# Optimization experiments

Hardware: AMD Instinct MI355X
Metric: run time of the kernel (lower is better)

## Reference

```python
import jax, jax.numpy as jnp
from jax import lax
import numpy as np

WINDOW_SIZES = (1, 2, 3)


def _proj(x, w1, b1, w2, b2):
    # gated projection: sigmoid(Linear1) * tanh(Linear2)
    return jax.nn.sigmoid(x @ w1.T + b1) * jnp.tanh(x @ w2.T + b2)


def setup_inputs() -> dict:
    key = jax.random.key(0)
    ks = jax.random.split(key, 16)
    V, E, D = 50000, 1024, 1024
    N, La, Lq = 64, 512, 64
    s = 0.02  # weight scale to keep sigmoid/tanh unsaturated
    return {
        "data_q": jax.random.randint(ks[0], (Lq,), 0, V),
        "data_as": jax.random.randint(ks[1], (N, La), 0, V),
        "emb": jax.random.normal(ks[2], (V, E), jnp.float32),
        "w1": jax.random.normal(ks[3], (D, E), jnp.float32) * s,
        "b1": jnp.zeros((D,), jnp.float32),
        "w2": jax.random.normal(ks[4], (D, E), jnp.float32) * s,
        "b2": jnp.zeros((D,), jnp.float32),
        "cw1": jax.random.normal(ks[5], (D, D, 1), jnp.float32) * s,
        "cb1": jnp.zeros((D,), jnp.float32),
        "cw2": jax.random.normal(ks[6], (D, D, 2), jnp.float32) * s,
        "cb2": jnp.zeros((D,), jnp.float32),
        "cw3": jax.random.normal(ks[7], (D, D, 3), jnp.float32) * s,
        "cb3": jnp.zeros((D,), jnp.float32),
        "lin_w": jax.random.normal(ks[8], (D, 3 * D), jnp.float32) * s,
        "lin_b": jnp.zeros((D,), jnp.float32),
        "soft_w": jax.random.normal(ks[9], (1, D), jnp.float32) * s,
        "soft_b": jnp.zeros((1,), jnp.float32),
    }


def reference(data_q, data_as, emb, w1, b1, w2, b2,
              cw1, cb1, cw2, cb2, cw3, cb3, lin_w, lin_b, soft_w, soft_b):
    N, La = data_as.shape
    a_tok = data_as.reshape(-1)                     # [T] concatenated answers
    emb_a = emb[a_tok]                              # [T, E]
    emb_q = emb[data_q]                             # [Lq, E]
    pa = _proj(emb_a, w1, b1, w2, b2)               # [T, D]
    pq = _proj(emb_q, w1, b1, w2, b2)               # [Lq, D]

    # attention: M_r = q @ a^T ; alpha = softmax over question positions
    M = pq @ pa.T                                   # [Lq, T]
    alpha = jax.nn.softmax(M.T, axis=1)             # [T, Lq]
    Y = alpha @ pq                                  # [T, D]
    sim = pa * Y                                    # elementwise compare (mul)

    starts = jnp.arange(N) * La
    x = sim.T[None]                                 # [1, D, T]
    pools = []
    for w, cw, cb in zip(WINDOW_SIZES, (cw1, cw2, cw3), (cb1, cb2, cb3)):
        conv = lax.conv_general_dilated(
            x, cw, (1,), 'VALID',
            dimension_numbers=('NCW', 'OIW', 'NCW'))[0].T + cb  # [T-w+1, D]
        conv = jax.nn.relu(conv)
        # DMax: per-answer max over rows [start_k, start_k + La - w + 1)
        idx = starts[:, None] + jnp.arange(La - w + 1)[None, :]  # [N, La-w+1]
        pools.append(conv[idx].max(axis=1))          # [N, D]

    cat = jnp.concatenate(pools, axis=1)            # [N, 3D]
    h = jnp.tanh(cat @ lin_w.T + lin_b)             # [N, D]
    logits = (h @ soft_w.T + soft_b).reshape(-1)    # [N]
    return jax.nn.log_softmax(logits)
```

## Files before the change

### kernel.cpp

```cpp
#include <hip/hip_runtime.h>

#define DEV __device__ __forceinline__

typedef __bf16 bf16x8 __attribute__((ext_vector_type(8)));
typedef float f32x4 __attribute__((ext_vector_type(4)));
typedef unsigned short u16;
typedef u16 u16x4 __attribute__((ext_vector_type(4)));

constexpr int T_ANS = 32768;
constexpr int LQ    = 64;
constexpr int M_ALL = T_ANS + LQ;
constexpr int M_PAD = 33024;
constexpr int DIM   = 1024;

DEV u16 f2bf(float x) {
  unsigned u = __float_as_uint(x);
  return (u16)((u + 0x7FFFu + ((u >> 16) & 1u)) >> 16);
}
DEV float bf2f(u16 s) { return __uint_as_float(((unsigned)s) << 16); }

DEV void gl2lds16(const void* g, void* l) {
  __builtin_amdgcn_global_load_lds(
      (const __attribute__((address_space(1))) unsigned int*)g,
      (__attribute__((address_space(3))) unsigned int*)l, 16, 0, 0);
}

#define MF(A, B, C) __builtin_amdgcn_mfma_f32_16x16x32_bf16(A, B, C, 0, 0, 0)


#define LFC(BASE, OFF) (*(const bf16x8*)((BASE) + (OFF)))

#define STG(G, LT, R0) gl2lds16((G) + (R0) * 2048 + gOff, (LT) + (R0) * 128 + tidOff)

#define MQUAD(Q, a00, a01, a10, a11)                                                  \
    acc[2*(Q)][0]   = MF(a00, bb00, acc[2*(Q)][0]);                                   \
    acc[2*(Q)][1]   = MF(a00, bb10, acc[2*(Q)][1]);                                   \
    acc[2*(Q)][2]   = MF(a00, bb20, acc[2*(Q)][2]);                                   \
    acc[2*(Q)][3]   = MF(a00, bb30, acc[2*(Q)][3]);                                   \
    acc[2*(Q)+1][0] = MF(a10, bb00, acc[2*(Q)+1][0]);                                 \
    acc[2*(Q)+1][1] = MF(a10, bb10, acc[2*(Q)+1][1]);                                 \
    acc[2*(Q)+1][2] = MF(a10, bb20, acc[2*(Q)+1][2]);                                 \
    acc[2*(Q)+1][3] = MF(a10, bb30, acc[2*(Q)+1][3]);                                 \
    acc[2*(Q)][0]   = MF(a01, bb01, acc[2*(Q)][0]);                                   \
    acc[2*(Q)][1]   = MF(a01, bb11, acc[2*(Q)][1]);                                   \
    acc[2*(Q)][2]   = MF(a01, bb21, acc[2*(Q)][2]);                                   \
    acc[2*(Q)][3]   = MF(a01, bb31, acc[2*(Q)][3]);                                   \
    acc[2*(Q)+1][0] = MF(a11, bb01, acc[2*(Q)+1][0]);                                 \
    acc[2*(Q)+1][1] = MF(a11, bb11, acc[2*(Q)+1][1]);                                 \
    acc[2*(Q)+1][2] = MF(a11, bb21, acc[2*(Q)+1][2]);                                 \
    acc[2*(Q)+1][3] = MF(a11, bb31, acc[2*(Q)+1][3]);

#define BARW                                                                          \
    __builtin_amdgcn_s_barrier();                                                     \
    asm volatile("s_waitcnt lgkmcnt(0)" ::: "memory");                                \
    __builtin_amdgcn_sched_barrier(0);

#define VM0 asm volatile("s_waitcnt vmcnt(0)" ::: "memory"); __builtin_amdgcn_sched_barrier(0);

#define TILE(Ac0, Ac1, Bc0, Bc1, S0, S1, VMWv)                                        \
  {                                                    \
    bb00 = LFC(Bc0, 0);    bb01 = LFC(Bc1, 0);                                        \
    bb10 = LFC(Bc0, 2048); bb11 = LFC(Bc1, 2048);                                     \
    bb20 = LFC(Bc0, 4096); bb21 = LFC(Bc1, 4096);                                     \
    bb30 = LFC(Bc0, 6144); bb31 = LFC(Bc1, 6144);                                     \
    bf16x8 a00 = LFC(Ac0, 0),    a01 = LFC(Ac1, 0);                                   \
    bf16x8 a10 = LFC(Ac0, 2048), a11 = LFC(Ac1, 2048);                                \
    S0                                                                                \
    asm volatile("s_waitcnt lgkmcnt(8)" ::: "memory");                                \
    BARW                                                                              \
    __builtin_amdgcn_s_setprio(1); MQUAD(0, a00, a01, a10, a11)                       \
    __builtin_amdgcn_s_setprio(0);                                                    \
    __builtin_amdgcn_s_barrier();                                                     \
  }                                                                                   \
  {                                                                          \
    bf16x8 a00 = LFC(Ac0, 4096), a01 = LFC(Ac1, 4096);                                \
    bf16x8 a10 = LFC(Ac0, 6144), a11 = LFC(Ac1, 6144);                                \
    S1                                                                                \
    BARW                                                                              \
    __builtin_amdgcn_s_setprio(1); MQUAD(1, a00, a01, a10, a11)                       \
    __builtin_amdgcn_s_setprio(0);                                                    \
    __builtin_amdgcn_s_barrier();                                                     \
  }                                                                                   \
  {                                                                          \
    bf16x8 a00 = LFC(Ac0, 8192),  a01 = LFC(Ac1, 8192);                               \
    bf16x8 a10 = LFC(Ac0, 10240), a11 = LFC(Ac1, 10240);                              \
    BARW                                                                              \
    __builtin_amdgcn_s_setprio(1); MQUAD(2, a00, a01, a10, a11)                       \
    __builtin_amdgcn_s_setprio(0);                                                    \
    __builtin_amdgcn_s_barrier();                                                     \
  }                                                                                   \
  {                                                                          \
    bf16x8 a00 = LFC(Ac0, 12288), a01 = LFC(Ac1, 12288);                              \
    bf16x8 a10 = LFC(Ac0, 14336), a11 = LFC(Ac1, 14336);                              \
    BARW                                                                              \
    __builtin_amdgcn_s_setprio(1); MQUAD(3, a00, a01, a10, a11)                       \
    __builtin_amdgcn_s_setprio(0);                                                    \
    VMWv                                                                              \
    __builtin_amdgcn_s_barrier();                                                     \
  }

#define S_A(G, LT) { const char* g_ = (G); STG(g_, LT, 0); STG(g_, LT, 64); STG(g_, LT, 128); STG(g_, LT, 192); }

#define GEMM_PIPE(KT)                                                                 \
  f32x4 acc[8][4] = {};                                                               \
  bf16x8 bb00, bb01, bb10, bb11, bb20, bb21, bb30, bb31;                              \
  const int e_ = lane & 7, h_ = lane >> 4, blk0 = (h_ ^ e_) << 4, blk1 = ((h_ ^ e_) ^ 4) << 4; \
  const int rA0 = (wm + lr) * 128, rB0 = (wn + lr) * 128;                             \
  const char* A0c0 = lds + rA0 + blk0;          const char* A0c1 = lds + rA0 + blk1;  \
  const char* B0c0 = lds + 32768 + rB0 + blk0;  const char* B0c1 = lds + 32768 + rB0 + blk1; \
  const char* A1c0 = lds + 65536 + rA0 + blk0;  const char* A1c1 = lds + 65536 + rA0 + blk1; \
  const char* B1c0 = lds + 98304 + rB0 + blk0;  const char* B1c1 = lds + 98304 + rB0 + blk1; \
  char* ldsA0 = lds;          char* ldsB0 = lds + 32768;                              \
  char* ldsA1 = lds + 65536;  char* ldsB1 = lds + 98304;                              \
  const int tidOff = tid * 16;                                                        \
  const int gOff = (tid >> 3) * 2048 + (((tid & 7) ^ ((tid >> 3) & 7)) << 4);         \
  S_A(Ab(0), ldsA0) S_A(Bb(0), ldsB0)                                                 \
  VM0                                                                                 \
  __builtin_amdgcn_s_barrier();                                                       \
  for (int kp = 0; kp < (KT) / 2 - 1; ++kp) {                                         \
    const int k1 = 2 * kp + 1;                                                        \
    TILE(A0c0, A0c1, B0c0, B0c1, S_A(Ab(k1), ldsA1), S_A(Bb(k1), ldsB1), VM0)         \
    TILE(A1c0, A1c1, B1c0, B1c1, S_A(Ab(k1 + 1), ldsA0), S_A(Bb(k1 + 1), ldsB0), VM0) \
  }                                                                                   \
  TILE(A0c0, A0c1, B0c0, B0c1, S_A(Ab((KT) - 1), ldsA1), S_A(Bb((KT) - 1), ldsB1), VM0) \
  TILE(A1c0, A1c1, B1c0, B1c1, , , )


__global__ void cast4(const float* __restrict__ src, u16* __restrict__ dst, int n4) {
  int i = blockIdx.x * 256 + threadIdx.x;
  if (i < n4) {
    float4 v = ((const float4*)src)[i];
    u16x4 o = { f2bf(v.x), f2bf(v.y), f2bf(v.z), f2bf(v.w) };
    ((u16x4*)dst)[i] = o;
  }
}

template<int W>
__global__ void cast_conv_w(const float* __restrict__ src, u16* __restrict__ dst) {
  int i = blockIdx.x * 256 + threadIdx.x;
  if (i < 1024 * 1024) {
#pragma unroll
    for (int k = 0; k < W; ++k)
      dst[(size_t)k * (1024 * 1024) + i] = f2bf(src[(size_t)i * W + k]);
  }
}

__global__ void pack_w12(const float* __restrict__ w1, const float* __restrict__ w2,
                         u16* __restrict__ W12) {
  int i = blockIdx.x * 256 + threadIdx.x;
  if (i < 2048 * 1024) {
    int n2 = i >> 10, k = i & 1023;
    int j = n2 >> 4, m = n2 & 15;
    const float* src = (j & 1) ? w2 : w1;
    W12[i] = f2bf(src[(size_t)((j >> 1) * 16 + m) * 1024 + k]);
  }
}

__global__ void gather_cast(const int* __restrict__ dq, const int* __restrict__ das,
                            const float* __restrict__ emb, u16* __restrict__ X) {
  const int row = blockIdx.x;
  const int c   = threadIdx.x;
  size_t dsto = (size_t)row * DIM + c * 4;
  if (row >= M_ALL) {
    u16x4 z = {0, 0, 0, 0};
    *(u16x4*)(X + dsto) = z;
    return;
  }
  const int tok = (row < T_ANS) ? das[row] : dq[row - T_ANS];
  float4 v = ((const float4*)(emb + (size_t)tok * DIM))[c];
  u16x4 o = { f2bf(v.x), f2bf(v.y), f2bf(v.z), f2bf(v.w) };
  *(u16x4*)(X + dsto) = o;
}

__global__ void transpose_pq(const u16* __restrict__ pa, u16* __restrict__ pqT) {
  int i = blockIdx.x * 256 + threadIdx.x;
  int e = i >> 6, q = i & 63;
  pqT[i] = pa[(size_t)(T_ANS + q) * DIM + e];
}

__global__ void zero_pad_sim(u16* __restrict__ sim) {
  int i = blockIdx.x * 256 + threadIdx.x;
  if (i < 2 * DIM) sim[(size_t)T_ANS * DIM + i] = 0;
}

__global__ void cast_cat(const float* __restrict__ cat, u16* __restrict__ catb) {
  int i = blockIdx.x * 256 + threadIdx.x;
  if (i < 128 * 3072) {
    int row = i / 3072;
    catb[i] = (row < 64) ? f2bf(cat[i]) : (u16)0;
  }
}


__global__ __launch_bounds__(512, 1)
void proj_g(const u16* __restrict__ X, const u16* __restrict__ W12,
            const float* __restrict__ b1, const float* __restrict__ b2,
            u16* __restrict__ pa) {
  extern __shared__ char lds[];
  const int tid = threadIdx.x, lane = tid & 63;
  const int wid = tid >> 6;
  const int wm = (wid >> 2) * 128, wn = (wid & 3) * 64;
  const int lr = lane & 15;
  const int wg = ((int)blockIdx.x % 8) * 129 + (int)blockIdx.x / 8;
  const int tm = (wg >> 3) * 256, tn = (wg & 7) * 256;
  const char* Ag = (const char*)X + (size_t)tm * 2048;
  const char* Bg = (const char*)W12 + (size_t)tn * 2048;
  auto Ab = [&](int kt) { return Ag + ((kt & 15) << 7); };
  auto Bb = [&](int kt) { return Bg + ((kt & 15) << 7); };

  GEMM_PIPE(16)

  u16* cw = (u16*)lds;
  const int lg = (lane >> 4) * 4;
#pragma unroll
  for (int pp = 0; pp < 2; ++pp) {
    const int clocal = ((wn >> 5) + pp) * 16 + lr;
    const int col = (tn >> 1) + clocal;
    const float b1v = b1[col], b2v = b2[col];
#pragma unroll
    for (int mi = 0; mi < 8; ++mi)
#pragma unroll
      for (int r = 0; r < 4; ++r) {
        const int rowL = wm + mi * 16 + lg + r;
        const float x1 = acc[mi][2 * pp][r] + b1v;
        const float x2 = acc[mi][2 * pp + 1][r] + b2v;
        const float sg = 1.f / (1.f + __expf(-x1));
        const float th = 2.f / (1.f + __expf(-2.f * x2)) - 1.f;
        cw[rowL * 132 + clocal] = f2bf(sg * th);
      }
  }
  __syncthreads();
#pragma unroll
  for (int it = 0; it < 16; ++it) {
    const int cid = it * 512 + tid;
    const int rowL = cid >> 5, c4 = (cid & 31) * 4;
    u16x4 v = *(const u16x4*)(cw + rowL * 132 + c4);
    *(u16x4*)(pa + (size_t)(tm + rowL) * DIM + (tn >> 1) + c4) = v;
  }
}


template<int W>
__global__ __launch_bounds__(512, 1)
void conv_g(const u16* __restrict__ sim, const u16* __restrict__ Bw,
            const float* __restrict__ cb, float* __restrict__ cat) {
  extern __shared__ char lds[];
  const int tid = threadIdx.x, lane = tid & 63;
  const int wid = tid >> 6;
  const int wm = (wid >> 2) * 128, wn = (wid & 3) * 64;
  const int lr = lane & 15;
  const int wg = ((int)blockIdx.x % 8) * 64 + (int)blockIdx.x / 8;
  const int tm = (wg >> 2) * 256, tn = (wg & 3) * 256;
  const char* Ag = (const char*)sim + (size_t)tm * 2048;
  const char* Bg = (const char*)Bw + (size_t)tn * 2048;
  auto Ab = [&](int kt) { return Ag + (kt >> 4) * 2048 + ((kt & 15) << 7); };
  auto Bb = [&](int kt) { return Bg + (size_t)(kt >> 4) * 2097152 + ((kt & 15) << 7); };

  GEMM_PIPE(16 * W)

  const int lg = (lane >> 4) * 4;
  const int n = tm >> 9;
#pragma unroll
  for (int ni = 0; ni < 4; ++ni) {
    const int col = tn + wn + ni * 16 + lr;
    const float cbv = cb[col];
    float vmax = 0.f;
#pragma unroll
    for (int mi = 0; mi < 8; ++mi)
#pragma unroll
      for (int r = 0; r < 4; ++r) {
        const int t = tm + wm + mi * 16 + lg + r;
        float v = fmaxf(acc[mi][ni][r] + cbv, 0.f);
        if ((t & 511) > 512 - W) v = 0.f;
        vmax = fmaxf(vmax, v);
      }
    vmax = fmaxf(vmax, __shfl_xor(vmax, 16));
    vmax = fmaxf(vmax, __shfl_xor(vmax, 32));
    if (lane < 16)
      atomicMax((int*)&cat[(size_t)n * 3072 + (W - 1) * 1024 + col], __float_as_int(vmax));
  }
}


__global__ __launch_bounds__(256, 2)
void attn_s(const u16* __restrict__ pa, float* __restrict__ Spart) {
  __shared__ alignas(16) u16 sA[128 * 32];
  __shared__ alignas(16) u16 sB[64 * 32];
  const int tid = threadIdx.x, lane = tid & 63;
  const int tm = blockIdx.x * 128;
  const int kbase = blockIdx.y * 256;
  const int wid = tid >> 6;
  const int wm = (wid >> 1) * 64, wn = (wid & 1) * 32;
  const u16* pq = pa + (size_t)T_ANS * DIM;
  f32x4 acc[4][2] = {};
  for (int k0 = kbase; k0 < kbase + 256; k0 += 32) {
#pragma unroll
    for (int j = 0; j < 2; ++j) {
      const int f = tid * 16 + j * 4096;
      const int r = f >> 6, cb = f & 63;
      gl2lds16((const char*)pa + (size_t)(tm + r) * 2048 + k0 * 2 + cb, (char*)sA + f);
    }
    {
      const int f = tid * 16;
      const int r = f >> 6, cb = f & 63;
      gl2lds16((const char*)pq + (size_t)r * 2048 + k0 * 2 + cb, (char*)sB + f);
    }
    __syncthreads();
    const int lr = lane & 15, lk = (lane >> 4) * 8;
    bf16x8 af[4], bfr[2];
#pragma unroll
    for (int i = 0; i < 4; ++i)
      af[i] = *(const bf16x8*)(sA + (wm + i * 16 + lr) * 32 + lk);
#pragma unroll
    for (int i = 0; i < 2; ++i)
      bfr[i] = *(const bf16x8*)(sB + (wn + i * 16 + lr) * 32 + lk);
#pragma unroll
    for (int mi = 0; mi < 4; ++mi)
#pragma unroll
      for (int ni = 0; ni < 2; ++ni)
        acc[mi][ni] = MF(af[mi], bfr[ni], acc[mi][ni]);
    __syncthreads();
  }
  const int lr = lane & 15, lg = (lane >> 4) * 4;
  float* Sp = Spart + (size_t)blockIdx.y * (T_ANS * 64);
#pragma unroll
  for (int mi = 0; mi < 4; ++mi)
#pragma unroll
    for (int ni = 0; ni < 2; ++ni)
#pragma unroll
      for (int r = 0; r < 4; ++r) {
        const int row = tm + wm + mi * 16 + lg + r;
        const int col = wn + ni * 16 + lr;
        Sp[(size_t)row * 64 + col] = acc[mi][ni][r];
      }
}

__global__ void softmax64(const float* __restrict__ Spart, u16* __restrict__ alpha) {
  const int row = blockIdx.x * 4 + (threadIdx.x >> 6);
  const int lane = threadIdx.x & 63;
  const size_t o = (size_t)row * 64 + lane;
  float v = Spart[o] + Spart[(size_t)1 * T_ANS * 64 + o]
          + Spart[(size_t)2 * T_ANS * 64 + o] + Spart[(size_t)3 * T_ANS * 64 + o];
  float m = v;
#pragma unroll
  for (int o2 = 32; o2 > 0; o2 >>= 1) m = fmaxf(m, __shfl_xor(m, o2));
  const float e = __expf(v - m);
  float s = e;
#pragma unroll
  for (int o2 = 32; o2 > 0; o2 >>= 1) s += __shfl_xor(s, o2);
  alpha[(size_t)row * 64 + lane] = f2bf(e / s);
}


__global__ __launch_bounds__(256, 2)
void attn_y_sim(const u16* __restrict__ alpha, const u16* __restrict__ pqT,
                const u16* __restrict__ pa, u16* __restrict__ sim) {
  __shared__ alignas(16) u16 sA[128 * 32];
  __shared__ alignas(16) u16 sB[128 * 32];
  const int tid = threadIdx.x, lane = tid & 63;
  const int tm = blockIdx.x * 128, tn = blockIdx.y * 128;
  const int wid = tid >> 6;
  const int wm = (wid >> 1) * 64, wn = (wid & 1) * 64;
  f32x4 acc[4][4] = {};
  for (int k0 = 0; k0 < 64; k0 += 32) {
#pragma unroll
    for (int j = 0; j < 2; ++j) {
      const int f = tid * 16 + j * 4096;
      const int r = f >> 6, cb = f & 63;
      gl2lds16((const char*)alpha + (size_t)(tm + r) * 128 + k0 * 2 + cb, (char*)sA + f);
      gl2lds16((const char*)pqT   + (size_t)(tn + r) * 128 + k0 * 2 + cb, (char*)sB + f);
    }
    __syncthreads();
    const int lr = lane & 15, lk = (lane >> 4) * 8;
    bf16x8 af[4], bfr[4];
#pragma unroll
    for (int i = 0; i < 4; ++i) {
      af[i]  = *(const bf16x8*)(sA + (wm + i * 16 + lr) * 32 + lk);
      bfr[i] = *(const bf16x8*)(sB + (wn + i * 16 + lr) * 32 + lk);
    }
#pragma unroll
    for (int mi = 0; mi < 4; ++mi)
#pragma unroll
      for (int ni = 0; ni < 4; ++ni)
        acc[mi][ni] = MF(af[mi], bfr[ni], acc[mi][ni]);
    __syncthreads();
  }
  const int lr = lane & 15, lg = (lane >> 4) * 4;
#pragma unroll
  for (int ni = 0; ni < 4; ++ni) {
    const int col = tn + wn + ni * 16 + lr;
#pragma unroll
    for (int mi = 0; mi < 4; ++mi)
#pragma unroll
      for (int r = 0; r < 4; ++r) {
        const int row = tm + wm + mi * 16 + lg + r;
        const size_t o = (size_t)row * DIM + col;
        sim[o] = f2bf(bf2f(pa[o]) * acc[mi][ni][r]);
      }
  }
}


__global__ __launch_bounds__(256, 2)
void final_h(const u16* __restrict__ catb, const u16* __restrict__ linb,
             const float* __restrict__ lin_b, float* __restrict__ h) {
  __shared__ alignas(16) u16 sA[128 * 32];
  __shared__ alignas(16) u16 sB[128 * 32];
  const int tid = threadIdx.x, lane = tid & 63;
  const int tn = blockIdx.y * 128;
  const int wid = tid >> 6;
  const int wm = (wid >> 1) * 64, wn = (wid & 1) * 64;
  f32x4 acc[4][4] = {};
  for (int k0 = 0; k0 < 3072; k0 += 32) {
#pragma unroll
    for (int j = 0; j < 2; ++j) {
      const int f = tid * 16 + j * 4096;
      const int r = f >> 6, cb = f & 63;
      gl2lds16((const char*)catb + (size_t)r * 6144 + k0 * 2 + cb, (char*)sA + f);
      gl2lds16((const char*)linb + (size_t)(tn + r) * 6144 + k0 * 2 + cb, (char*)sB + f);
    }
    __syncthreads();
    const int lr = lane & 15, lk = (lane >> 4) * 8;
    bf16x8 af[4], bfr[4];
#pragma unroll
    for (int i = 0; i < 4; ++i) {
      af[i]  = *(const bf16x8*)(sA + (wm + i * 16 + lr) * 32 + lk);
      bfr[i] = *(const bf16x8*)(sB + (wn + i * 16 + lr) * 32 + lk);
    }
#pragma unroll
    for (int mi = 0; mi < 4; ++mi)
#pragma unroll
      for (int ni = 0; ni < 4; ++ni)
        acc[mi][ni] = MF(af[mi], bfr[ni], acc[mi][ni]);
    __syncthreads();
  }
  const int lr = lane & 15, lg = (lane >> 4) * 4;
#pragma unroll
  for (int ni = 0; ni < 4; ++ni) {
    const int col = tn + wn + ni * 16 + lr;
    const float bv = lin_b[col];
#pragma unroll
    for (int mi = 0; mi < 4; ++mi)
#pragma unroll
      for (int r = 0; r < 4; ++r) {
        const int row = wm + mi * 16 + lg + r;
        if (row < 64) {
          const float x = acc[mi][ni][r] + bv;
          h[(size_t)row * DIM + col] = 2.f / (1.f + __expf(-2.f * x)) - 1.f;
        }
      }
  }
}

__global__ void final_logits(const float* __restrict__ h, const float* __restrict__ soft_w,
                             const float* __restrict__ soft_b, float* __restrict__ out) {
  __shared__ float part[256];
  const int t = threadIdx.x;
  const int n = t >> 2, q = t & 3;
  float s = 0.f;
  for (int j = q * 256; j < q * 256 + 256; ++j) s += h[(size_t)n * DIM + j] * soft_w[j];
  part[t] = s;
  __syncthreads();
  if (t < 64) {
    float logit = part[t * 4] + part[t * 4 + 1] + part[t * 4 + 2] + part[t * 4 + 3] + soft_b[0];
    float m = logit;
#pragma unroll
    for (int o = 32; o > 0; o >>= 1) m = fmaxf(m, __shfl_xor(m, o));
    float e = __expf(logit - m);
    float ssum = e;
#pragma unroll
    for (int o = 32; o > 0; o >>= 1) ssum += __shfl_xor(ssum, o);
    out[t] = (logit - m) - logf(ssum);
  }
}


extern "C" void kernel_launch(void* const* d_in, const int* in_sizes, int n_in,
                              void* d_out, int out_size, void* d_ws, size_t ws_size,
                              hipStream_t stream) {
  const int*   data_q  = (const int*)d_in[0];
  const int*   data_as = (const int*)d_in[1];
  const float* emb     = (const float*)d_in[2];
  const float* w1      = (const float*)d_in[3];
  const float* b1      = (const float*)d_in[4];
  const float* w2      = (const float*)d_in[5];
  const float* b2      = (const float*)d_in[6];
  const float* cw1     = (const float*)d_in[7];
  const float* cb1     = (const float*)d_in[8];
  const float* cw2     = (const float*)d_in[9];
  const float* cb2     = (const float*)d_in[10];
  const float* cw3     = (const float*)d_in[11];
  const float* cb3     = (const float*)d_in[12];
  const float* lin_w   = (const float*)d_in[13];
  const float* lin_b   = (const float*)d_in[14];
  const float* soft_w  = (const float*)d_in[15];
  const float* soft_b  = (const float*)d_in[16];
  float* out = (float*)d_out;

  hipFuncSetAttribute((const void*)proj_g, hipFuncAttributeMaxDynamicSharedMemorySize, 131072);
  hipFuncSetAttribute((const void*)conv_g<1>, hipFuncAttributeMaxDynamicSharedMemorySize, 131072);
  hipFuncSetAttribute((const void*)conv_g<2>, hipFuncAttributeMaxDynamicSharedMemorySize, 131072);
  hipFuncSetAttribute((const void*)conv_g<3>, hipFuncAttributeMaxDynamicSharedMemorySize, 131072);

  u16* X     = (u16*)d_ws;
  u16* pa    = X    + (size_t)M_PAD * DIM;
  u16* W12   = pa   + (size_t)M_PAD * DIM;
  u16* cwb   = W12  + (size_t)2 * 1024 * 1024;
  u16* linb  = cwb  + (size_t)6 * 1024 * 1024;
  u16* pqT   = linb + (size_t)3 * 1024 * 1024;
  u16* alpha = pqT  + 64 * 1024;
  float* cat = (float*)(alpha + (size_t)T_ANS * 64);
  u16* catb  = (u16*)(cat + 64 * 3072);
  float* h   = (float*)(catb + 128 * 3072);
  u16* simb  = X;
  float* Spart = (float*)X;

  hipMemsetAsync(cat, 0, 64 * 3072 * sizeof(float), stream);

  pack_w12<<<8192, 256, 0, stream>>>(w1, w2, W12);
  cast4<<<3072, 256, 0, stream>>>(lin_w, linb, 3072 * 1024 / 4);
  cast_conv_w<1><<<4096, 256, 0, stream>>>(cw1, cwb);
  cast_conv_w<2><<<4096, 256, 0, stream>>>(cw2, cwb + (size_t)1 * 1024 * 1024);
  cast_conv_w<3><<<4096, 256, 0, stream>>>(cw3, cwb + (size_t)3 * 1024 * 1024);

  gather_cast<<<M_PAD, 256, 0, stream>>>(data_q, data_as, emb, X);

  proj_g<<<1032, 512, 131072, stream>>>(X, W12, b1, b2, pa);
  transpose_pq<<<256, 256, 0, stream>>>(pa, pqT);

  attn_s<<<dim3(T_ANS / 128, 4), 256, 0, stream>>>(pa, Spart);
  softmax64<<<T_ANS / 4, 256, 0, stream>>>(Spart, alpha);
  attn_y_sim<<<dim3(T_ANS / 128, 8), 256, 0, stream>>>(alpha, pqT, pa, simb);
  zero_pad_sim<<<8, 256, 0, stream>>>(simb);

  conv_g<1><<<512, 512, 131072, stream>>>(simb, cwb, cb1, cat);
  conv_g<2><<<512, 512, 131072, stream>>>(simb, cwb + (size_t)1 * 1024 * 1024, cb2, cat);
  conv_g<3><<<512, 512, 131072, stream>>>(simb, cwb + (size_t)3 * 1024 * 1024, cb3, cat);

  cast_cat<<<1536, 256, 0, stream>>>(cat, catb);
  final_h<<<dim3(1, 8), 256, 0, stream>>>(catb, linb, lin_b, h);
  final_logits<<<1, 256, 0, stream>>>(h, soft_w, soft_b, out);
}
```

Baseline: 763.1 us.

## Replace double-buffered K=64 GEMM pipeline with 4-stage K=32 ring buffer

Rewrites the shared GEMM main loop used by the projection and conv kernels. K-tiles shrink from 64 to 32 and rotate through four LDS buffers, with global-to-LDS loads issued two tiles ahead and waited on with vmcnt(4) instead of draining to zero. One barrier per tile replaces the sub-phase barriers and priority toggles. The aim is deeper memory latency hiding and less synchronisation, at the cost of twice as many K iterations with fewer MFMAs per barrier and a changed LDS swizzle.

```diff
diff --git a/kernel.cpp b/kernel.cpp
--- a/kernel.cpp
+++ b/kernel.cpp
@@ -26,104 +26,72 @@
 }
 
 #define MF(A, B, C) __builtin_amdgcn_mfma_f32_16x16x32_bf16(A, B, C, 0, 0, 0)
-
-
-#define LFC(BASE, OFF) (*(const bf16x8*)((BASE) + (OFF)))
-
-#define STG(G, LT, R0) gl2lds16((G) + (R0) * 2048 + gOff, (LT) + (R0) * 128 + tidOff)
-
-#define MQUAD(Q, a00, a01, a10, a11)                                                  \
-    acc[2*(Q)][0]   = MF(a00, bb00, acc[2*(Q)][0]);                                   \
-    acc[2*(Q)][1]   = MF(a00, bb10, acc[2*(Q)][1]);                                   \
-    acc[2*(Q)][2]   = MF(a00, bb20, acc[2*(Q)][2]);                                   \
-    acc[2*(Q)][3]   = MF(a00, bb30, acc[2*(Q)][3]);                                   \
-    acc[2*(Q)+1][0] = MF(a10, bb00, acc[2*(Q)+1][0]);                                 \
-    acc[2*(Q)+1][1] = MF(a10, bb10, acc[2*(Q)+1][1]);                                 \
-    acc[2*(Q)+1][2] = MF(a10, bb20, acc[2*(Q)+1][2]);                                 \
-    acc[2*(Q)+1][3] = MF(a10, bb30, acc[2*(Q)+1][3]);                                 \
-    acc[2*(Q)][0]   = MF(a01, bb01, acc[2*(Q)][0]);                                   \
-    acc[2*(Q)][1]   = MF(a01, bb11, acc[2*(Q)][1]);                                   \
-    acc[2*(Q)][2]   = MF(a01, bb21, acc[2*(Q)][2]);                                   \
-    acc[2*(Q)][3]   = MF(a01, bb31, acc[2*(Q)][3]);                                   \
-    acc[2*(Q)+1][0] = MF(a11, bb01, acc[2*(Q)+1][0]);                                 \
-    acc[2*(Q)+1][1] = MF(a11, bb11, acc[2*(Q)+1][1]);                                 \
-    acc[2*(Q)+1][2] = MF(a11, bb21, acc[2*(Q)+1][2]);                                 \
-    acc[2*(Q)+1][3] = MF(a11, bb31, acc[2*(Q)+1][3]);
-
-#define BARW                                                                          \
-    __builtin_amdgcn_s_barrier();                                                     \
-    asm volatile("s_waitcnt lgkmcnt(0)" ::: "memory");                                \
-    __builtin_amdgcn_sched_barrier(0);
-
-#define VM0 asm volatile("s_waitcnt vmcnt(0)" ::: "memory"); __builtin_amdgcn_sched_barrier(0);
-
-#define TILE(Ac0, Ac1, Bc0, Bc1, S0, S1, VMWv)                                        \
-  {                                                    \
-    bb00 = LFC(Bc0, 0);    bb01 = LFC(Bc1, 0);                                        \
-    bb10 = LFC(Bc0, 2048); bb11 = LFC(Bc1, 2048);                                     \
-    bb20 = LFC(Bc0, 4096); bb21 = LFC(Bc1, 4096);                                     \
-    bb30 = LFC(Bc0, 6144); bb31 = LFC(Bc1, 6144);                                     \
-    bf16x8 a00 = LFC(Ac0, 0),    a01 = LFC(Ac1, 0);                                   \
-    bf16x8 a10 = LFC(Ac0, 2048), a11 = LFC(Ac1, 2048);                                \
-    S0                                                                                \
-    asm volatile("s_waitcnt lgkmcnt(8)" ::: "memory");                                \
-    BARW                                                                              \
-    __builtin_amdgcn_s_setprio(1); MQUAD(0, a00, a01, a10, a11)                       \
-    __builtin_amdgcn_s_setprio(0);                                                    \
-    __builtin_amdgcn_s_barrier();                                                     \
+#define LFC(P, OFF) (*(const bf16x8*)((P) + (OFF)))
+
+
+#define STG(G, LT, R0) gl2lds16((G) + (R0) * 2048 + gOff, (LT) + (R0) * 64 + ldOff)
+
+#define S_TILE(AT, BT, BUF)                                                           \
+  { const char* ga_ = (AT); const char* gb_ = (BT); char* lb_ = (BUF);                \
+    STG(ga_, lb_, 0); STG(ga_, lb_, 128);                                             \
+    STG(gb_, lb_ + 16384, 0); STG(gb_, lb_ + 16384, 128); }
+
+#define VMC4 asm volatile("s_waitcnt vmcnt(4)" ::: "memory");
+#define VMC0 asm volatile("s_waitcnt vmcnt(0)" ::: "memory");
+
+#define TILEV3(BUF, STAGES, WAIT)                                                     \
+  {                                                                                   \
+    STAGES                                                                            \
+    const char* Ar = (BUF) + rdA;                                                     \
+    const char* Br = (BUF) + 16384 + rdB;                                             \
+    bf16x8 a0 = LFC(Ar, 0),    a1 = LFC(Ar, 1024), a2 = LFC(Ar, 2048), a3 = LFC(Ar, 3072); \
+    bf16x8 a4 = LFC(Ar, 4096), a5 = LFC(Ar, 5120), a6 = LFC(Ar, 6144), a7 = LFC(Ar, 7168); \
+    bf16x8 c0 = LFC(Br, 0), c1 = LFC(Br, 1024), c2 = LFC(Br, 2048), c3 = LFC(Br, 3072);    \
+    acc[0][0] = MF(a0, c0, acc[0][0]); acc[0][1] = MF(a0, c1, acc[0][1]);             \
+    acc[0][2] = MF(a0, c2, acc[0][2]); acc[0][3] = MF(a0, c3, acc[0][3]);             \
+    acc[1][0] = MF(a1, c0, acc[1][0]); acc[1][1] = MF(a1, c1, acc[1][1]);             \
+    acc[1][2] = MF(a1, c2, acc[1][2]); acc[1][3] = MF(a1, c3, acc[1][3]);             \
+    acc[2][0] = MF(a2, c0, acc[2][0]); acc[2][1] = MF(a2, c1, acc[2][1]);             \
+    acc[2][2] = MF(a2, c2, acc[2][2]); acc[2][3] = MF(a2, c3, acc[2][3]);             \
+    acc[3][0] = MF(a3, c0, acc[3][0]); acc[3][1] = MF(a3, c1, acc[3][1]);             \
+    acc[3][2] = MF(a3, c2, acc[3][2]); acc[3][3] = MF(a3, c3, acc[3][3]);             \
+    acc[4][0] = MF(a4, c0, acc[4][0]); acc[4][1] = MF(a4, c1, acc[4][1]);             \
+    acc[4][2] = MF(a4, c2, acc[4][2]); acc[4][3] = MF(a4, c3, acc[4][3]);             \
+    acc[5][0] = MF(a5, c0, acc[5][0]); acc[5][1] = MF(a5, c1, acc[5][1]);             \
+    acc[5][2] = MF(a5, c2, acc[5][2]); acc[5][3] = MF(a5, c3, acc[5][3]);             \
+    acc[6][0] = MF(a6, c0, acc[6][0]); acc[6][1] = MF(a6, c1, acc[6][1]);             \
+    acc[6][2] = MF(a6, c2, acc[6][2]); acc[6][3] = MF(a6, c3, acc[6][3]);             \
+    acc[7][0] = MF(a7, c0, acc[7][0]); acc[7][1] = MF(a7, c1, acc[7][1]);             \
+    acc[7][2] = MF(a7, c2, acc[7][2]); acc[7][3] = MF(a7, c3, acc[7][3]);             \
+    WAIT                                                                              \
+    asm volatile("s_barrier" ::: "memory");                                           \
+  }
+
+#define GEMM_V3(NT)                                                                   \
+  f32x4 acc[8][4] = {};                                                               \
+  const int ldOff = tid * 16;                                                         \
+  const int gOff = (tid >> 2) * 2048 + (((tid & 3) ^ ((tid >> 2) & 3)) << 4);         \
+  const int blk_ = (((lane >> 4) ^ (lane & 3)) << 4);                                 \
+  const int rdA = (wm + (lane & 15)) * 64 + blk_;                                     \
+  const int rdB = (wn + (lane & 15)) * 64 + blk_;                                     \
+  char* b0_ = lds; char* b1_ = lds + 32768; char* b2_ = lds + 65536; char* b3_ = lds + 98304; \
+  S_TILE(Ab(0), Bb(0), b0_) S_TILE(Ab(1), Bb(1), b1_)                                 \
+  VMC4                                                                                \
+  asm volatile("s_barrier" ::: "memory");                                             \
+  for (int g = 0; g < (NT) / 4 - 1; ++g) {                                            \
+    const int t = 4 * g;                                                              \
+    TILEV3(b0_, S_TILE(Ab(t + 2), Bb(t + 2), b2_), VMC4)                              \
+    TILEV3(b1_, S_TILE(Ab(t + 3), Bb(t + 3), b3_), VMC4)                              \
+    TILEV3(b2_, S_TILE(Ab(t + 4), Bb(t + 4), b0_), VMC4)                              \
+    TILEV3(b3_, S_TILE(Ab(t + 5), Bb(t + 5), b1_), VMC4)                              \
   }                                                                                   \
-  {                                                                          \
-    bf16x8 a00 = LFC(Ac0, 4096), a01 = LFC(Ac1, 4096);                                \
-    bf16x8 a10 = LFC(Ac0, 6144), a11 = LFC(Ac1, 6144);                                \
-    S1                                                                                \
-    BARW                                                                              \
-    __builtin_amdgcn_s_setprio(1); MQUAD(1, a00, a01, a10, a11)                       \
-    __builtin_amdgcn_s_setprio(0);                                                    \
-    __builtin_amdgcn_s_barrier();                                                     \
-  }                                                                                   \
-  {                                                                          \
-    bf16x8 a00 = LFC(Ac0, 8192),  a01 = LFC(Ac1, 8192);                               \
-    bf16x8 a10 = LFC(Ac0, 10240), a11 = LFC(Ac1, 10240);                              \
-    BARW                                                                              \
-    __builtin_amdgcn_s_setprio(1); MQUAD(2, a00, a01, a10, a11)                       \
-    __builtin_amdgcn_s_setprio(0);                                                    \
-    __builtin_amdgcn_s_barrier();                                                     \
-  }                                                                                   \
-  {                                                                          \
-    bf16x8 a00 = LFC(Ac0, 12288), a01 = LFC(Ac1, 12288);                              \
-    bf16x8 a10 = LFC(Ac0, 14336), a11 = LFC(Ac1, 14336);                              \
-    BARW                                                                              \
-    __builtin_amdgcn_s_setprio(1); MQUAD(3, a00, a01, a10, a11)                       \
-    __builtin_amdgcn_s_setprio(0);                                                    \
-    VMWv                                                                              \
-    __builtin_amdgcn_s_barrier();                                                     \
-  }
-
-#define S_A(G, LT) { const char* g_ = (G); STG(g_, LT, 0); STG(g_, LT, 64); STG(g_, LT, 128); STG(g_, LT, 192); }
-
-#define GEMM_PIPE(KT)                                                                 \
-  f32x4 acc[8][4] = {};                                                               \
-  bf16x8 bb00, bb01, bb10, bb11, bb20, bb21, bb30, bb31;                              \
-  const int e_ = lane & 7, h_ = lane >> 4, blk0 = (h_ ^ e_) << 4, blk1 = ((h_ ^ e_) ^ 4) << 4; \
-  const int rA0 = (wm + lr) * 128, rB0 = (wn + lr) * 128;                             \
-  const char* A0c0 = lds + rA0 + blk0;          const char* A0c1 = lds + rA0 + blk1;  \
-  const char* B0c0 = lds + 32768 + rB0 + blk0;  const char* B0c1 = lds + 32768 + rB0 + blk1; \
-  const char* A1c0 = lds + 65536 + rA0 + blk0;  const char* A1c1 = lds + 65536 + rA0 + blk1; \
-  const char* B1c0 = lds + 98304 + rB0 + blk0;  const char* B1c1 = lds + 98304 + rB0 + blk1; \
-  char* ldsA0 = lds;          char* ldsB0 = lds + 32768;                              \
-  char* ldsA1 = lds + 65536;  char* ldsB1 = lds + 98304;                              \
-  const int tidOff = tid * 16;                                                        \
-  const int gOff = (tid >> 3) * 2048 + (((tid & 7) ^ ((tid >> 3) & 7)) << 4);         \
-  S_A(Ab(0), ldsA0) S_A(Bb(0), ldsB0)                                                 \
-  VM0                                                                                 \
-  __builtin_amdgcn_s_barrier();                                                       \
-  for (int kp = 0; kp < (KT) / 2 - 1; ++kp) {                                         \
-    const int k1 = 2 * kp + 1;                                                        \
-    TILE(A0c0, A0c1, B0c0, B0c1, S_A(Ab(k1), ldsA1), S_A(Bb(k1), ldsB1), VM0)         \
-    TILE(A1c0, A1c1, B1c0, B1c1, S_A(Ab(k1 + 1), ldsA0), S_A(Bb(k1 + 1), ldsB0), VM0) \
-  }                                                                                   \
-  TILE(A0c0, A0c1, B0c0, B0c1, S_A(Ab((KT) - 1), ldsA1), S_A(Bb((KT) - 1), ldsB1), VM0) \
-  TILE(A1c0, A1c1, B1c0, B1c1, , , )
+  {                                                                                   \
+    const int t = (NT) - 4;                                                           \
+    TILEV3(b0_, S_TILE(Ab(t + 2), Bb(t + 2), b2_), VMC4)                              \
+    TILEV3(b1_, S_TILE(Ab(t + 3), Bb(t + 3), b3_), VMC4)                              \
+    TILEV3(b2_, , VMC0)                                                               \
+    TILEV3(b3_, , )                                                                   \
+  }
 
 
 __global__ void cast4(const float* __restrict__ src, u16* __restrict__ dst, int n4) {
@@ -205,10 +173,10 @@
   const int tm = (wg >> 3) * 256, tn = (wg & 7) * 256;
   const char* Ag = (const char*)X + (size_t)tm * 2048;
   const char* Bg = (const char*)W12 + (size_t)tn * 2048;
-  auto Ab = [&](int kt) { return Ag + ((kt & 15) << 7); };
-  auto Bb = [&](int kt) { return Bg + ((kt & 15) << 7); };
-
-  GEMM_PIPE(16)
+  auto Ab = [&](int t) { return Ag + (t << 6); };
+  auto Bb = [&](int t) { return Bg + (t << 6); };
+
+  GEMM_V3(32)
 
   u16* cw = (u16*)lds;
   const int lg = (lane >> 4) * 4;
@@ -253,10 +221,10 @@
   const int tm = (wg >> 2) * 256, tn = (wg & 3) * 256;
   const char* Ag = (const char*)sim + (size_t)tm * 2048;
   const char* Bg = (const char*)Bw + (size_t)tn * 2048;
-  auto Ab = [&](int kt) { return Ag + (kt >> 4) * 2048 + ((kt & 15) << 7); };
-  auto Bb = [&](int kt) { return Bg + (size_t)(kt >> 4) * 2097152 + ((kt & 15) << 7); };
-
-  GEMM_PIPE(16 * W)
+  auto Ab = [&](int t) { return Ag + (t >> 5) * 2048 + ((t & 31) << 6); };
+  auto Bb = [&](int t) { return Bg + (size_t)(t >> 5) * 2097152 + ((t & 31) << 6); };
+
+  GEMM_V3(32 * W)
 
   const int lg = (lane >> 4) * 4;
   const int n = tm >> 9;
```

Result: no change. 773.4 us (+1.3%).
